# Performance work log

Measured on AMD Instinct MI355X. Metric: run time of the kernel, lower is better.

The kernel has to match this reference:

```python
import jax, jax.numpy as jnp
import numpy as np

N, D, IN, OUT, K = 50000, 16, 256, 128, 4  # nodes, sampled degree, input_size, output_size, heads
LEAKY_SLOPE = 0.01  # torch F.leaky_relu default


def setup_inputs() -> dict:
    key = jax.random.key(0)
    k1, k2, k3, k4 = jax.random.split(key, 4)
    X = jax.random.normal(k1, (N, IN), dtype=jnp.float32)
    W = jax.random.normal(k2, (K, OUT, IN), dtype=jnp.float32) * 0.05
    a = jax.random.normal(k3, (K, 2 * OUT), dtype=jnp.float32) * 0.05
    neighbor_idx = jax.random.randint(k4, (N, D), 0, N)  # fixed-degree neighbor sample
    return {"X": X, "W": W, "a": a, "neighbor_idx": neighbor_idx}


def reference(X, W, a, neighbor_idx):
    # X: [N, IN]; W: [K, OUT, IN]; a: [K, 2*OUT]; neighbor_idx: [N, D]
    out_dim = W.shape[1]
    # Per-head linear map of every node once: Wh[k, n] = W[k] @ X[n]
    Wh = jnp.einsum('koi,ni->kno', W, X)                       # [K, N, OUT]
    # a splits: first OUT weights multiply mapped neighbour, second OUT multiply mapped self
    a_nb, a_self = a[:, :out_dim], a[:, out_dim:]
    e_nb = jnp.einsum('kno,ko->kn', Wh, a_nb)                  # [K, N] score contribution as a neighbour
    e_self = jnp.einsum('kno,ko->kn', Wh, a_self)              # [K, N] score contribution as center node
    # Edge logits: e[k, i, d] = leaky_relu(a_nb.Wh[j] + a_self.Wh[i]), j = neighbor_idx[i, d]
    e = jax.nn.leaky_relu(e_nb[:, neighbor_idx] + e_self[:, :, None], LEAKY_SLOPE)  # [K, N, D]
    alpha = jax.nn.softmax(e, axis=-1)                         # softmax over each node's neighbour set
    Wh_nb = jnp.take(Wh, neighbor_idx, axis=1)                 # [K, N, D, OUT] gathered neighbour features
    h = jnp.einsum('knd,kndo->kno', alpha, Wh_nb)              # [K, N, OUT] attention-weighted aggregate
    # Concatenate heads along feature dim, matching per-node head-concat in the torch loop
    return jnp.transpose(h, (1, 0, 2)).reshape(X.shape[0], -1)  # [N, K*OUT]
```

## Files before the change

### kernel.cpp

```cpp
#include <hip/hip_runtime.h>

#define N_NODES 50000
#define D_NB 16
#define IN_DIM 256
#define OUT_DIM 128
#define K_HEADS 4
#define SLOPE 0.01f
#define NSLICE 16
#define SLICE_COLS 32

typedef __attribute__((ext_vector_type(8))) short short8;
typedef __attribute__((ext_vector_type(4))) float f32x4;

static __device__ __forceinline__ unsigned f2bf(float f) {
    unsigned u = __float_as_uint(f);
    unsigned r = u + 0x7fffu + ((u >> 16) & 1u);
    return r >> 16;
}
static __device__ __forceinline__ float bf2f(unsigned short b) {
    return __uint_as_float(((unsigned)b) << 16);
}

__global__ void wb_kernel(const float* __restrict__ W, unsigned short* __restrict__ Wb) {
    int id = blockIdx.x * blockDim.x + threadIdx.x;
    if (id < K_HEADS * OUT_DIM * IN_DIM) Wb[id] = (unsigned short)f2bf(W[id]);
}

__global__ __launch_bounds__(256) void wt8_kernel(
    const float* __restrict__ W, const float* __restrict__ a, float* __restrict__ wt8)
{
    const int i = threadIdx.x;
    #pragma unroll
    for (int k = 0; k < K_HEADS; ++k) {
        float s0 = 0.f, s1 = 0.f;
        for (int o = 0; o < OUT_DIM; ++o) {
            const float w = W[((size_t)k * OUT_DIM + o) * IN_DIM + i];
            s0 += w * a[k * 2 * OUT_DIM + o];
            s1 += w * a[k * 2 * OUT_DIM + OUT_DIM + o];
        }
        wt8[(k * 2 + 0) * IN_DIM + i] = s0;
        wt8[(k * 2 + 1) * IN_DIM + i] = s1;
    }
}

__global__ __launch_bounds__(256) void prep_kernel(
    const float* __restrict__ X, const float* __restrict__ wt8,
    unsigned short* __restrict__ Xb, float* __restrict__ e_nb, float* __restrict__ e_self)
{
    const int t = threadIdx.x;
    const int w = t >> 6;
    const int lane = t & 63;
    const int n = blockIdx.x * 4 + w;

    const float4 x = *(const float4*)(X + (size_t)n * IN_DIM + lane * 4);
    uint2 pk;
    pk.x = f2bf(x.x) | (f2bf(x.y) << 16);
    pk.y = f2bf(x.z) | (f2bf(x.w) << 16);
    *(uint2*)(Xb + (size_t)n * IN_DIM + lane * 4) = pk;

    float p[8];
    #pragma unroll
    for (int v = 0; v < 8; ++v) {
        const float4 wv = *(const float4*)(wt8 + v * IN_DIM + lane * 4);
        p[v] = x.x * wv.x + x.y * wv.y + x.z * wv.z + x.w * wv.w;
    }
    #pragma unroll
    for (int sh = 32; sh >= 1; sh >>= 1) {
        #pragma unroll
        for (int v = 0; v < 8; ++v) p[v] += __shfl_xor(p[v], sh);
    }
    if (lane < 8) {
        const int k = lane >> 1;
        float* dst = (lane & 1) ? e_self : e_nb;
        dst[(size_t)k * N_NODES + n] = p[lane];
    }
}

__global__ __launch_bounds__(256) void agg_kernel(
    const int* __restrict__ nidx, const unsigned short* __restrict__ Xb,
    const float* __restrict__ e_nb, const float* __restrict__ e_self,
    unsigned short* __restrict__ aggX, int n0, int nc)
{
    const int t = threadIdx.x;
    const int w = t >> 6;
    const int lane = t & 63;
    const int n = n0 + blockIdx.x * 4 + w;
    if (n >= n0 + nc || n >= N_NODES) return;

    const int k = lane >> 4;
    const int dl = lane & 15;

    const int nbr = nidx[(size_t)n * D_NB + dl];
    const float x = e_nb[(size_t)k * N_NODES + nbr] + e_self[(size_t)k * N_NODES + n];
    const float v = x > 0.f ? x : SLOPE * x;
    float m = v;
    #pragma unroll
    for (int sh = 8; sh >= 1; sh >>= 1) m = fmaxf(m, __shfl_xor(m, sh, 16));
    const float pz = __expf(v - m);
    float sum = pz;
    #pragma unroll
    for (int sh = 8; sh >= 1; sh >>= 1) sum += __shfl_xor(sum, sh, 16);
    const float alpha = pz / sum;

    float acc[4][4] = {};
    #pragma unroll
    for (int h = 0; h < 2; ++h) {
        uint2 u[8];
        #pragma unroll
        for (int b = 0; b < 8; ++b) {
            const int nd = __shfl(nbr, h * 8 + b);
            u[b] = *(const uint2*)(Xb + (size_t)nd * IN_DIM + lane * 4);
        }
        #pragma unroll
        for (int b = 0; b < 8; ++b) {
            const float x0 = bf2f((unsigned short)(u[b].x & 0xffffu));
            const float x1 = bf2f((unsigned short)(u[b].x >> 16));
            const float x2 = bf2f((unsigned short)(u[b].y & 0xffffu));
            const float x3 = bf2f((unsigned short)(u[b].y >> 16));
            #pragma unroll
            for (int kk = 0; kk < 4; ++kk) {
                const float ad = __shfl(alpha, kk * 16 + h * 8 + b);
                acc[kk][0] += ad * x0;
                acc[kk][1] += ad * x1;
                acc[kk][2] += ad * x2;
                acc[kk][3] += ad * x3;
            }
        }
    }
    #pragma unroll
    for (int kk = 0; kk < 4; ++kk) {
        uint2 pk;
        pk.x = f2bf(acc[kk][0]) | (f2bf(acc[kk][1]) << 16);
        pk.y = f2bf(acc[kk][2]) | (f2bf(acc[kk][3]) << 16);
        *(uint2*)(aggX + ((size_t)kk * nc + (n - n0)) * IN_DIM + lane * 4) = pk;
    }
}

__global__ __launch_bounds__(256) void gemm2_kernel(
    const unsigned short* __restrict__ aggX, const unsigned short* __restrict__ Wb,
    float* __restrict__ out, int n0, int nc)
{
    __shared__ unsigned short Wlds[2][SLICE_COLS * IN_DIM];

    const int t = threadIdx.x;
    const int lane = t & 63;
    const int w = t >> 6;
    const int lrow = lane & 15;
    const int lk = lane >> 4;
    const int m0 = n0 + blockIdx.x * 64 + w * 16;

    const int arow = m0 + lrow;
    const bool avalid = (arow < n0 + nc) && (arow < N_NODES);

    auto STAGE = [&](int st, int buf) {
        const unsigned short* WbS = Wb + (size_t)st * SLICE_COLS * IN_DIM;
        #pragma unroll
        for (int i = 0; i < 4; ++i) {
            const int c = i * 256 + t;
            const int r = c >> 5;
            const int p = c & 31;
            const int cu = p ^ (r & 7);
            const unsigned short* gsrc = WbS + r * IN_DIM + cu * 8;
            unsigned short* ldst = &Wlds[buf][c * 8];
            __builtin_amdgcn_global_load_lds(
                (const __attribute__((address_space(1))) void*)gsrc,
                (__attribute__((address_space(3))) void*)ldst, 16, 0, 0);
        }
    };

    short8 af[8];
    STAGE(0, 0);
    __syncthreads();

    for (int st = 0; st < NSLICE; ++st) {
        const int buf = st & 1;
        if (st + 1 < NSLICE) STAGE(st + 1, buf ^ 1);

        if ((st & 3) == 0) {
            const unsigned short* Ar = aggX
                + ((size_t)(st >> 2) * nc + (arow - n0)) * IN_DIM + lk * 8;
            #pragma unroll
            for (int kk = 0; kk < 8; ++kk)
                af[kk] = avalid ? *(const short8*)(Ar + kk * 32)
                                : short8{0, 0, 0, 0, 0, 0, 0, 0};
        }

        f32x4 acc[2] = {};
        #pragma unroll
        for (int kk = 0; kk < 8; ++kk) {
            #pragma unroll
            for (int nt = 0; nt < 2; ++nt) {
                const int row = nt * 16 + lrow;
                const int pos = (kk * 4 + lk) ^ (row & 7);
                const short8 bf = *(const short8*)(&Wlds[buf][row * IN_DIM + pos * 8]);
                acc[nt] = __builtin_amdgcn_mfma_f32_16x16x32_bf16(bf, af[kk], acc[nt], 0, 0, 0);
            }
        }

        const int k = st >> 2, cb = st & 3;
        if (avalid) {
            #pragma unroll
            for (int nt = 0; nt < 2; ++nt) {
                *(f32x4*)(out + (size_t)arow * (K_HEADS * OUT_DIM)
                          + k * OUT_DIM + cb * SLICE_COLS + nt * 16 + lk * 4) = acc[nt];
            }
        }
        __syncthreads();
    }
}

extern "C" void kernel_launch(void* const* d_in, const int* in_sizes, int n_in,
                              void* d_out, int out_size, void* d_ws, size_t ws_size,
                              hipStream_t stream) {
    const float* X = (const float*)d_in[0];
    const float* W = (const float*)d_in[1];
    const float* a = (const float*)d_in[2];
    const int* nidx = (const int*)d_in[3];
    float* out = (float*)d_out;

    const size_t WbB  = (size_t)K_HEADS * OUT_DIM * IN_DIM * 2;
    const size_t XbB  = (size_t)N_NODES * IN_DIM * 2;
    const size_t wt8B = (size_t)8 * IN_DIM * 4;
    const size_t eB   = (size_t)K_HEADS * N_NODES * 4;
    auto need = [&](int nc) {
        return WbB + XbB + wt8B + 2 * eB + (size_t)K_HEADS * nc * IN_DIM * 2 + 1024;
    };

    int np, nc;
    if      (ws_size >= need(50000)) { np = 1; nc = 50000; }
    else if (ws_size >= need(25000)) { np = 2; nc = 25000; }
    else                             { np = 4; nc = 12500; }

    char* p = (char*)d_ws;
    unsigned short* Wb   = (unsigned short*)p;   p += WbB;
    unsigned short* Xb   = (unsigned short*)p;   p += XbB;
    float*          wt8  = (float*)p;            p += wt8B;
    float*          enb  = (float*)p;            p += eB;
    float*          esf  = (float*)p;            p += eB;
    unsigned short* aggX = (unsigned short*)p;

    hipLaunchKernelGGL(wb_kernel,
        dim3((K_HEADS * OUT_DIM * IN_DIM + 255) / 256), dim3(256), 0, stream, W, Wb);

    hipLaunchKernelGGL(wt8_kernel, dim3(1), dim3(256), 0, stream, W, a, wt8);

    hipLaunchKernelGGL(prep_kernel,
        dim3(N_NODES / 4), dim3(256), 0, stream, X, wt8, Xb, enb, esf);

    for (int pass = 0; pass < np; ++pass) {
        const int nb0 = pass * nc;
        hipLaunchKernelGGL(agg_kernel,
            dim3((nc + 3) / 4), dim3(256), 0, stream, nidx, Xb, enb, esf, aggX, nb0, nc);
        hipLaunchKernelGGL(gemm2_kernel,
            dim3((nc + 63) / 64), dim3(256), 0, stream, aggX, Wb, out, nb0, nc);
    }
}
```

Before: 177.1 us.

## Merge weight-prep kernels, double GEMM rows per block, add nontemporal memory ops

```diff
diff --git a/kernel.cpp b/kernel.cpp
--- a/kernel.cpp
+++ b/kernel.cpp
@@ -11,6 +11,7 @@
 
 typedef __attribute__((ext_vector_type(8))) short short8;
 typedef __attribute__((ext_vector_type(4))) float f32x4;
+typedef __attribute__((ext_vector_type(2))) unsigned u32x2;
 
 static __device__ __forceinline__ unsigned f2bf(float f) {
     unsigned u = __float_as_uint(f);
@@ -21,14 +22,15 @@
     return __uint_as_float(((unsigned)b) << 16);
 }
 
-__global__ void wb_kernel(const float* __restrict__ W, unsigned short* __restrict__ Wb) {
-    int id = blockIdx.x * blockDim.x + threadIdx.x;
-    if (id < K_HEADS * OUT_DIM * IN_DIM) Wb[id] = (unsigned short)f2bf(W[id]);
-}
-
-__global__ __launch_bounds__(256) void wt8_kernel(
-    const float* __restrict__ W, const float* __restrict__ a, float* __restrict__ wt8)
-{
+__global__ __launch_bounds__(256) void prep_w_kernel(
+    const float* __restrict__ W, const float* __restrict__ a,
+    unsigned short* __restrict__ Wb, float* __restrict__ wt8)
+{
+    if (blockIdx.x < 2048) {
+        const int id = blockIdx.x * 256 + threadIdx.x;
+        Wb[id] = (unsigned short)f2bf(W[id]);
+        return;
+    }
     const int i = threadIdx.x;
     #pragma unroll
     for (int k = 0; k < K_HEADS; ++k) {
@@ -52,17 +54,18 @@
     const int lane = t & 63;
     const int n = blockIdx.x * 4 + w;
 
-    const float4 x = *(const float4*)(X + (size_t)n * IN_DIM + lane * 4);
+    const f32x4 x = __builtin_nontemporal_load(
+        (const f32x4*)(X + (size_t)n * IN_DIM + lane * 4));
     uint2 pk;
-    pk.x = f2bf(x.x) | (f2bf(x.y) << 16);
-    pk.y = f2bf(x.z) | (f2bf(x.w) << 16);
+    pk.x = f2bf(x[0]) | (f2bf(x[1]) << 16);
+    pk.y = f2bf(x[2]) | (f2bf(x[3]) << 16);
     *(uint2*)(Xb + (size_t)n * IN_DIM + lane * 4) = pk;
 
     float p[8];
     #pragma unroll
     for (int v = 0; v < 8; ++v) {
         const float4 wv = *(const float4*)(wt8 + v * IN_DIM + lane * 4);
-        p[v] = x.x * wv.x + x.y * wv.y + x.z * wv.z + x.w * wv.w;
+        p[v] = x[0] * wv.x + x[1] * wv.y + x[2] * wv.z + x[3] * wv.w;
     }
     #pragma unroll
     for (int sh = 32; sh >= 1; sh >>= 1) {
@@ -90,7 +93,7 @@
     const int k = lane >> 4;
     const int dl = lane & 15;
 
-    const int nbr = nidx[(size_t)n * D_NB + dl];
+    const int nbr = __builtin_nontemporal_load(nidx + (size_t)n * D_NB + dl);
     const float x = e_nb[(size_t)k * N_NODES + nbr] + e_self[(size_t)k * N_NODES + n];
     const float v = x > 0.f ? x : SLOPE * x;
     float m = v;
@@ -129,10 +132,11 @@
     }
     #pragma unroll
     for (int kk = 0; kk < 4; ++kk) {
-        uint2 pk;
-        pk.x = f2bf(acc[kk][0]) | (f2bf(acc[kk][1]) << 16);
-        pk.y = f2bf(acc[kk][2]) | (f2bf(acc[kk][3]) << 16);
-        *(uint2*)(aggX + ((size_t)kk * nc + (n - n0)) * IN_DIM + lane * 4) = pk;
+        u32x2 pk;
+        pk[0] = f2bf(acc[kk][0]) | (f2bf(acc[kk][1]) << 16);
+        pk[1] = f2bf(acc[kk][2]) | (f2bf(acc[kk][3]) << 16);
+        __builtin_nontemporal_store(pk,
+            (u32x2*)(aggX + ((size_t)kk * nc + (n - n0)) * IN_DIM + lane * 4));
     }
 }
 
@@ -147,10 +151,12 @@
     const int w = t >> 6;
     const int lrow = lane & 15;
     const int lk = lane >> 4;
-    const int m0 = n0 + blockIdx.x * 64 + w * 16;
-
-    const int arow = m0 + lrow;
-    const bool avalid = (arow < n0 + nc) && (arow < N_NODES);
+    const int m0 = n0 + blockIdx.x * 128 + w * 16;
+
+    const int arow0 = m0 + lrow;
+    const int arow1 = arow0 + 64;
+    const bool av0 = (arow0 < n0 + nc) && (arow0 < N_NODES);
+    const bool av1 = (arow1 < n0 + nc) && (arow1 < N_NODES);
 
     auto STAGE = [&](int st, int buf) {
         const unsigned short* WbS = Wb + (size_t)st * SLICE_COLS * IN_DIM;
@@ -168,7 +174,7 @@
         }
     };
 
-    short8 af[8];
+    short8 af0[8], af1[8];
     STAGE(0, 0);
     __syncthreads();
 
@@ -177,15 +183,19 @@
         if (st + 1 < NSLICE) STAGE(st + 1, buf ^ 1);
 
         if ((st & 3) == 0) {
-            const unsigned short* Ar = aggX
-                + ((size_t)(st >> 2) * nc + (arow - n0)) * IN_DIM + lk * 8;
+            const size_t hb = (size_t)(st >> 2) * nc;
+            const unsigned short* Ar0 = aggX + (hb + (arow0 - n0)) * IN_DIM + lk * 8;
+            const unsigned short* Ar1 = aggX + (hb + (arow1 - n0)) * IN_DIM + lk * 8;
             #pragma unroll
-            for (int kk = 0; kk < 8; ++kk)
-                af[kk] = avalid ? *(const short8*)(Ar + kk * 32)
-                                : short8{0, 0, 0, 0, 0, 0, 0, 0};
-        }
-
-        f32x4 acc[2] = {};
+            for (int kk = 0; kk < 8; ++kk) {
+                af0[kk] = av0 ? __builtin_nontemporal_load((const short8*)(Ar0 + kk * 32))
+                              : short8{0, 0, 0, 0, 0, 0, 0, 0};
+                af1[kk] = av1 ? __builtin_nontemporal_load((const short8*)(Ar1 + kk * 32))
+                              : short8{0, 0, 0, 0, 0, 0, 0, 0};
+            }
+        }
+
+        f32x4 acc0[2] = {}, acc1[2] = {};
         #pragma unroll
         for (int kk = 0; kk < 8; ++kk) {
             #pragma unroll
@@ -193,17 +203,19 @@
                 const int row = nt * 16 + lrow;
                 const int pos = (kk * 4 + lk) ^ (row & 7);
                 const short8 bf = *(const short8*)(&Wlds[buf][row * IN_DIM + pos * 8]);
-                acc[nt] = __builtin_amdgcn_mfma_f32_16x16x32_bf16(bf, af[kk], acc[nt], 0, 0, 0);
+                acc0[nt] = __builtin_amdgcn_mfma_f32_16x16x32_bf16(bf, af0[kk], acc0[nt], 0, 0, 0);
+                acc1[nt] = __builtin_amdgcn_mfma_f32_16x16x32_bf16(bf, af1[kk], acc1[nt], 0, 0, 0);
             }
         }
 
         const int k = st >> 2, cb = st & 3;
-        if (avalid) {
-            #pragma unroll
-            for (int nt = 0; nt < 2; ++nt) {
-                *(f32x4*)(out + (size_t)arow * (K_HEADS * OUT_DIM)
-                          + k * OUT_DIM + cb * SLICE_COLS + nt * 16 + lk * 4) = acc[nt];
-            }
+        const size_t cbase = (size_t)k * OUT_DIM + cb * SLICE_COLS + lk * 4;
+        #pragma unroll
+        for (int nt = 0; nt < 2; ++nt) {
+            if (av0) __builtin_nontemporal_store(acc0[nt],
+                (f32x4*)(out + (size_t)arow0 * (K_HEADS * OUT_DIM) + cbase + nt * 16));
+            if (av1) __builtin_nontemporal_store(acc1[nt],
+                (f32x4*)(out + (size_t)arow1 * (K_HEADS * OUT_DIM) + cbase + nt * 16));
         }
         __syncthreads();
     }
@@ -239,10 +251,7 @@
     float*          esf  = (float*)p;            p += eB;
     unsigned short* aggX = (unsigned short*)p;
 
-    hipLaunchKernelGGL(wb_kernel,
-        dim3((K_HEADS * OUT_DIM * IN_DIM + 255) / 256), dim3(256), 0, stream, W, Wb);
-
-    hipLaunchKernelGGL(wt8_kernel, dim3(1), dim3(256), 0, stream, W, a, wt8);
+    hipLaunchKernelGGL(prep_w_kernel, dim3(2049), dim3(256), 0, stream, W, a, Wb, wt8);
 
     hipLaunchKernelGGL(prep_kernel,
         dim3(N_NODES / 4), dim3(256), 0, stream, X, wt8, Xb, enb, esf);
@@ -252,6 +261,6 @@
         hipLaunchKernelGGL(agg_kernel,
             dim3((nc + 3) / 4), dim3(256), 0, stream, nidx, Xb, enb, esf, aggX, nb0, nc);
         hipLaunchKernelGGL(gemm2_kernel,
-            dim3((nc + 63) / 64), dim3(256), 0, stream, aggX, Wb, out, nb0, nc);
-    }
-}
+            dim3((nc + 127) / 128), dim3(256), 0, stream, aggX, Wb, out, nb0, nc);
+    }
+}
```

Result: slower. 190.1 us (+7.4%).
